# Kernel tuning notes

Measured on AMD Instinct MI355X. Metric: run time of the kernel, lower is better.

The kernel has to match this reference:

```python
import jax, jax.numpy as jnp
import numpy as np

TAU = 1.0      # temperature for gumbel-softmax
EPS = 1e-12    # F.normalize eps


def _l2norm(v, axis):
    n = jnp.sqrt(jnp.sum(v * v, axis=axis, keepdims=True))
    return v / jnp.maximum(n, EPS)


def setup_inputs() -> dict:
    key = jax.random.key(0)
    k1, k2, k3, k4 = jax.random.split(key, 4)
    b, c, h, w, n = 8, 512, 64, 64, 1024
    x = jax.random.normal(k1, (b, c, h, w), dtype=jnp.float32)
    centers = jax.random.normal(k2, (n, c), dtype=jnp.float32)          # VQ codebook
    clusters = jax.random.normal(k3, (n, c), dtype=jnp.float32)         # ClusterLookup param
    gumbel_noise = jax.random.gumbel(k4, (b, n, h, w), dtype=jnp.float32)
    return {"x": x, "centers": centers, "clusters": clusters, "gumbel_noise": gumbel_noise}


def reference(x, centers, clusters, gumbel_noise):
    # similarity logits: [b, n, h, w]
    inner = jnp.einsum('bchw,nc->bnhw', x, centers)
    # hard gumbel-softmax (straight-through) over code dim
    y_soft = jax.nn.softmax((inner + gumbel_noise) / TAU, axis=1)
    idx = jnp.argmax(y_soft, axis=1)                                     # [b, h, w]
    y_hard = jax.nn.one_hot(idx, centers.shape[0], axis=1, dtype=y_soft.dtype)
    one_hot = y_hard - jax.lax.stop_gradient(y_soft) + y_soft            # [b, n, h, w]
    # quantized features: codebook lookup expressed as einsum
    z_q = jnp.einsum('bnhw,nd->bdhw', one_hot, centers)                  # [b, c, h, w]
    # ClusterLookup(z_q, alpha=None, is_direct=False)
    nf = _l2norm(z_q, axis=1)
    ncl = _l2norm(clusters, axis=1)
    ip = jnp.einsum('bchw,nc->bnhw', nf, ncl)                            # cluster logits
    preds = jnp.argmax(ip, axis=1)                                       # [b, h, w] int
    probs = jax.nn.one_hot(preds, clusters.shape[0], axis=1, dtype=ip.dtype)
    cluster_loss = -jnp.mean(jnp.sum(probs * ip, axis=1))
    return (cluster_loss, preds, ip, z_q)
```

## Files before the change

### kernel.cpp

```cpp
#include <hip/hip_runtime.h>
#include <math.h>

#define C 512
#define HW 4096
#define N 1024
#define NPIX 32768
#define MARGIN 2.0f

typedef short s16x8 __attribute__((ext_vector_type(8)));
typedef float f32x4 __attribute__((ext_vector_type(4)));

__device__ inline unsigned short f2bf(float f) {
    unsigned int u = __float_as_uint(f);
    return (unsigned short)((u + 0x7FFFu + ((u >> 16) & 1u)) >> 16);
}
__device__ inline float h2f(unsigned short u) {
    _Float16 h; __builtin_memcpy(&h, &u, 2); return (float)h;
}
__device__ inline unsigned short f2h(float f) {
    _Float16 h = (_Float16)f; unsigned short u; __builtin_memcpy(&u, &h, 2); return u;
}
__device__ inline unsigned int mono(float v) {
    unsigned int u = __float_as_uint(v);
    return (u & 0x80000000u) ? ~u : (u | 0x80000000u);
}
__device__ inline void gload_lds16(const void* gsrc, void* ldst) {
    __builtin_amdgcn_global_load_lds(
        (const __attribute__((address_space(1))) unsigned int*)gsrc,
        (__attribute__((address_space(3))) unsigned int*)ldst, 16, 0, 0);
}

__global__ __launch_bounds__(64) void k_norms(const float* __restrict__ centers,
                                              const float* __restrict__ clusters,
                                              float* __restrict__ cnorm,
                                              float* __restrict__ clnorm) {
    int r = blockIdx.x;
    const float* src = (r < N) ? (centers + (size_t)r * C) : (clusters + (size_t)(r - N) * C);
    int lane = threadIdx.x;
    float s = 0.f;
    for (int k = lane; k < C; k += 64) { float v = src[k]; s += v * v; }
    #pragma unroll
    for (int m = 1; m < 64; m <<= 1) s += __shfl_xor(s, m, 64);
    if (lane == 0) {
        float nrm = sqrtf(s);
        if (nrm < 1e-12f) nrm = 1e-12f;
        if (r < N) cnorm[r] = nrm; else clnorm[r - N] = nrm;
    }
}

__global__ __launch_bounds__(256) void k_gemmM(const float* __restrict__ centers,
                                               const float* __restrict__ clusters,
                                               const float* __restrict__ cnorm,
                                               const float* __restrict__ clnorm,
                                               float* __restrict__ M) {
    __shared__ float as[32][68];
    __shared__ float bs[32][68];
    int tid = threadIdx.x;
    int tx = tid & 15, ty = tid >> 4;
    int i0 = blockIdx.x * 64, j0 = blockIdx.y * 64;
    int lrow = tid >> 2, lkq = (tid & 3) * 8;
    float acc[4][4] = {};
    for (int kc = 0; kc < C; kc += 32) {
        float4 a0 = *(const float4*)(centers + (size_t)(i0 + lrow) * C + kc + lkq);
        float4 a1 = *(const float4*)(centers + (size_t)(i0 + lrow) * C + kc + lkq + 4);
        float4 b0 = *(const float4*)(clusters + (size_t)(j0 + lrow) * C + kc + lkq);
        float4 b1 = *(const float4*)(clusters + (size_t)(j0 + lrow) * C + kc + lkq + 4);
        __syncthreads();
        as[lkq+0][lrow]=a0.x; as[lkq+1][lrow]=a0.y; as[lkq+2][lrow]=a0.z; as[lkq+3][lrow]=a0.w;
        as[lkq+4][lrow]=a1.x; as[lkq+5][lrow]=a1.y; as[lkq+6][lrow]=a1.z; as[lkq+7][lrow]=a1.w;
        bs[lkq+0][lrow]=b0.x; bs[lkq+1][lrow]=b0.y; bs[lkq+2][lrow]=b0.z; bs[lkq+3][lrow]=b0.w;
        bs[lkq+4][lrow]=b1.x; bs[lkq+5][lrow]=b1.y; bs[lkq+6][lrow]=b1.z; bs[lkq+7][lrow]=b1.w;
        __syncthreads();
        #pragma unroll
        for (int k = 0; k < 32; k += 4) {
            float av[4][4], bv[4][4];
            #pragma unroll
            for (int kk = 0; kk < 4; ++kk) {
                float4 ta = *(const float4*)&as[k+kk][tx*4];
                float4 tb = *(const float4*)&bs[k+kk][ty*4];
                av[kk][0]=ta.x; av[kk][1]=ta.y; av[kk][2]=ta.z; av[kk][3]=ta.w;
                bv[kk][0]=tb.x; bv[kk][1]=tb.y; bv[kk][2]=tb.z; bv[kk][3]=tb.w;
            }
            #pragma unroll
            for (int kk = 0; kk < 4; ++kk)
                #pragma unroll
                for (int ii = 0; ii < 4; ++ii)
                    #pragma unroll
                    for (int jj = 0; jj < 4; ++jj)
                        acc[ii][jj] = fmaf(av[kk][ii], bv[kk][jj], acc[ii][jj]);
        }
    }
    float rci[4], rcj[4];
    #pragma unroll
    for (int ii = 0; ii < 4; ++ii) rci[ii] = cnorm[i0 + tx*4 + ii];
    #pragma unroll
    for (int jj = 0; jj < 4; ++jj) rcj[jj] = clnorm[j0 + ty*4 + jj];
    #pragma unroll
    for (int ii = 0; ii < 4; ++ii)
        #pragma unroll
        for (int jj = 0; jj < 4; ++jj)
            M[(size_t)(i0 + tx*4 + ii) * N + (j0 + ty*4 + jj)] = acc[ii][jj] / (rci[ii] * rcj[jj]);
}

__global__ __launch_bounds__(256) void k_rowstat(const float* __restrict__ M,
                                                 float* __restrict__ rowmax,
                                                 int* __restrict__ rowarg) {
    __shared__ float sv[256];
    __shared__ int   sa[256];
    int i = blockIdx.x, tid = threadIdx.x;
    float bv = -INFINITY; int ba = 0;
    for (int j = tid; j < N; j += 256) {
        float v = M[(size_t)i * N + j];
        if (v > bv || (v == bv && j < ba)) { bv = v; ba = j; }
    }
    sv[tid] = bv; sa[tid] = ba;
    __syncthreads();
    for (int s = 128; s > 0; s >>= 1) {
        if (tid < s) {
            float v = sv[tid + s]; int a = sa[tid + s];
            if (v > sv[tid] || (v == sv[tid] && a < sa[tid])) { sv[tid] = v; sa[tid] = a; }
        }
        __syncthreads();
    }
    if (tid == 0) { rowmax[i] = sv[0]; rowarg[i] = sa[0]; }
}

__global__ __launch_bounds__(256) void k_prepT(const float* __restrict__ x,
                                               float* __restrict__ xT) {
    __shared__ float t[64][65];
    int bidx = blockIdx.x;
    int pt = bidx & 63, kt = (bidx >> 6) & 7, b = bidx >> 9;
    int r = threadIdx.x >> 4, c4 = (threadIdx.x & 15) * 4;
    const float* src = x + ((size_t)b * C + kt * 64) * HW + pt * 64;
    #pragma unroll
    for (int rr = 0; rr < 4; ++rr) {
        int row = rr * 16 + r;
        float4 v = *(const float4*)(src + (size_t)row * HW + c4);
        t[row][c4] = v.x; t[row][c4+1] = v.y; t[row][c4+2] = v.z; t[row][c4+3] = v.w;
    }
    __syncthreads();
    float* dst = xT + ((size_t)b * HW + pt * 64) * C + kt * 64;
    #pragma unroll
    for (int rr = 0; rr < 4; ++rr) {
        int row = rr * 16 + r;
        float4 v = { t[c4][row], t[c4+1][row], t[c4+2][row], t[c4+3][row] };
        *(float4*)(dst + (size_t)row * C + c4) = v;
    }
}

__global__ __launch_bounds__(64) void k_cenfrag(const float* __restrict__ centers,
                                                unsigned short* __restrict__ cenB) {
    int f = blockIdx.x;
    int nt = f >> 4, kt = f & 15;
    int lane = threadIdx.x;
    int r = lane & 15, g = lane >> 4;
    const float* src = centers + (size_t)(nt * 16 + r) * C + kt * 32 + g * 4;
    float4 lo = *(const float4*)src;
    float4 hi = *(const float4*)(src + 16);
    union { unsigned short us[8]; uint4 q; } u;
    u.us[0]=f2bf(lo.x); u.us[1]=f2bf(lo.y); u.us[2]=f2bf(lo.z); u.us[3]=f2bf(lo.w);
    u.us[4]=f2bf(hi.x); u.us[5]=f2bf(hi.y); u.us[6]=f2bf(hi.z); u.us[7]=f2bf(hi.w);
    *(uint4*)(cenB + ((size_t)f * 64 + lane) * 8) = u.q;
}

__global__ __launch_bounds__(256, 3) void k_fused(const float* __restrict__ xT,
                                                  const unsigned short* __restrict__ cenB,
                                                  const float* __restrict__ gumbel,
                                                  const float* __restrict__ centers,
                                                  int* __restrict__ idxb) {
    __shared__ unsigned short cen[2][8192];
    __shared__ unsigned long long pixkey[64];
    __shared__ unsigned int candlist[4][256];
    __shared__ int candcount[4];

    int tid = threadIdx.x;
    int lane = tid & 63, w = tid >> 6;
    int r = lane & 15, g = lane >> 4;

    int p0 = blockIdx.x * 64;
    int b = p0 >> 12, hw0 = p0 & (HW - 1);

    if (tid < 64) pixkey[tid] = 0ull;
    if (tid < 4) candcount[tid] = 0;

    {
        const char* src = (const char*)cenB + w * 4096 + lane * 16;
        char* dst = (char*)&cen[0][0] + w * 4096;
        #pragma unroll
        for (int i = 0; i < 4; ++i) gload_lds16(src + i * 1024, dst + i * 1024);
    }

    s16x8 a[16];
    {
        const float* xrow = xT + (size_t)(p0 + w * 16 + r) * C;
        #pragma unroll
        for (int kt = 0; kt < 16; ++kt) {
            float4 lo = *(const float4*)(xrow + kt * 32 + g * 4);
            float4 hi = *(const float4*)(xrow + kt * 32 + 16 + g * 4);
            s16x8 t;
            t[0]=(short)f2bf(lo.x); t[1]=(short)f2bf(lo.y); t[2]=(short)f2bf(lo.z); t[3]=(short)f2bf(lo.w);
            t[4]=(short)f2bf(hi.x); t[5]=(short)f2bf(hi.y); t[6]=(short)f2bf(hi.z); t[7]=(short)f2bf(hi.w);
            a[kt] = t;
        }
    }
    __syncthreads();

    const float* gpx = gumbel + (size_t)b * N * HW + hw0 + w * 16 + g * 4;
    float m4[4] = {-INFINITY, -INFINITY, -INFINITY, -INFINITY};
    int cur = 0;

    for (int tc = 0; tc < 8; ++tc) {
        unsigned int keepH[16];
        #pragma unroll
        for (int s = 0; s < 8; ++s) {
            int t = tc * 8 + s;
            if (t < 63) {
                const char* src = (const char*)cenB + (size_t)(t + 1) * 16384 + w * 4096 + lane * 16;
                char* dst = (char*)&cen[cur ^ 1][0] + w * 4096;
                #pragma unroll
                for (int i = 0; i < 4; ++i) gload_lds16(src + i * 1024, dst + i * 1024);
            }
            float4 gv = *(const float4*)(gpx + (size_t)(t * 16 + r) * HW);
            const s16x8* bp = (const s16x8*)&cen[cur][0] + lane;
            f32x4 acc0 = {0.f,0.f,0.f,0.f}, acc1 = {0.f,0.f,0.f,0.f};
            #pragma unroll
            for (int kt = 0; kt < 16; kt += 2) {
                acc0 = __builtin_amdgcn_mfma_f32_16x16x32_bf16(a[kt],   bp[kt*64],     acc0, 0,0,0);
                acc1 = __builtin_amdgcn_mfma_f32_16x16x32_bf16(a[kt+1], bp[(kt+1)*64], acc1, 0,0,0);
            }
            float v0 = acc0[0]+acc1[0]+gv.x, v1 = acc0[1]+acc1[1]+gv.y;
            float v2 = acc0[2]+acc1[2]+gv.z, v3 = acc0[3]+acc1[3]+gv.w;
            m4[0]=fmaxf(m4[0],v0); m4[1]=fmaxf(m4[1],v1);
            m4[2]=fmaxf(m4[2],v2); m4[3]=fmaxf(m4[3],v3);
            keepH[s*2]   = (unsigned int)f2h(v0) | ((unsigned int)f2h(v1) << 16);
            keepH[s*2+1] = (unsigned int)f2h(v2) | ((unsigned int)f2h(v3) << 16);
            __syncthreads();
            cur ^= 1;
        }
        #pragma unroll
        for (int s2 = 1; s2 < 16; s2 <<= 1) {
            #pragma unroll
            for (int j = 0; j < 4; ++j) m4[j] = fmaxf(m4[j], __shfl_xor(m4[j], s2, 64));
        }
        float thr[4];
        #pragma unroll
        for (int j = 0; j < 4; ++j) thr[j] = m4[j] - MARGIN;
        #pragma unroll
        for (int s = 0; s < 8; ++s) {
            int nn = ((tc * 8 + s) << 4) + r;
            #pragma unroll
            for (int j2 = 0; j2 < 2; ++j2) {
                unsigned int pk = keepH[s * 2 + j2];
                float lo = h2f((unsigned short)(pk & 0xFFFFu));
                float hi = h2f((unsigned short)(pk >> 16));
                if (lo >= thr[j2 * 2]) {
                    int pos = atomicAdd(&candcount[w], 1);
                    if (pos < 256) candlist[w][pos] =
                        (unsigned int)nn | ((unsigned int)(w * 16 + g * 4 + j2 * 2) << 10);
                }
                if (hi >= thr[j2 * 2 + 1]) {
                    int pos = atomicAdd(&candcount[w], 1);
                    if (pos < 256) candlist[w][pos] =
                        (unsigned int)nn | ((unsigned int)(w * 16 + g * 4 + j2 * 2 + 1) << 10);
                }
            }
        }
    }

    int cc = candcount[w]; if (cc > 256) cc = 256;
    int sl = lane & 15, cg = lane >> 4;
    for (int t0 = 0; t0 < cc; t0 += 4) {
        int c = t0 + cg;
        bool valid = c < cc;
        unsigned int e = candlist[w][valid ? c : 0];
        int n = (int)(e & 1023u), pl = (int)(e >> 10);
        const float* xr = xT + (size_t)(p0 + pl) * C;
        const float* cenr = centers + (size_t)n * C;
        float s = 0.f;
        #pragma unroll
        for (int m = 0; m < 8; ++m) {
            int G = sl + (m << 4);
            float4 xv = *(const float4*)(xr + (G << 2));
            float4 cv = *(const float4*)(cenr + (G << 2));
            s = fmaf(xv.x, cv.x, s); s = fmaf(xv.y, cv.y, s);
            s = fmaf(xv.z, cv.z, s); s = fmaf(xv.w, cv.w, s);
        }
        #pragma unroll
        for (int s2 = 1; s2 < 16; s2 <<= 1) s += __shfl_xor(s, s2, 64);
        if (valid && sl == 0) {
            float val = s + gumbel[((size_t)b * N + n) * HW + hw0 + pl];
            unsigned long long key = ((unsigned long long)mono(val) << 32) | (unsigned int)(1023 - n);
            atomicMax(&pixkey[pl], key);
        }
    }
    __syncthreads();
    if (tid < 64) idxb[p0 + tid] = 1023 - (int)(unsigned int)(pixkey[tid] & 0xFFFFFFFFull);
}

__global__ __launch_bounds__(256) void k_preds(const int* __restrict__ idxb,
                                               const float* __restrict__ rowmax,
                                               const int* __restrict__ rowarg,
                                               float* __restrict__ preds_out,
                                               float* __restrict__ partial) {
    __shared__ float sv[256];
    int gid = blockIdx.x * 256 + threadIdx.x;
    int i = idxb[gid];
    preds_out[gid] = (float)rowarg[i];
    sv[threadIdx.x] = rowmax[i];
    __syncthreads();
    for (int s = 128; s > 0; s >>= 1) {
        if (threadIdx.x < s) sv[threadIdx.x] += sv[threadIdx.x + s];
        __syncthreads();
    }
    if (threadIdx.x == 0) partial[blockIdx.x] = sv[0];
}

__global__ __launch_bounds__(256) void k_gather(const float* __restrict__ src, int ncols,
                                                const int* __restrict__ idx,
                                                float* __restrict__ dst) {
    __shared__ float rows[64][65];
    int tile = blockIdx.x;
    int col0 = blockIdx.y * 64;
    int tid = threadIdx.x;
    int lane = tid & 63, w = tid >> 6;
    int b = tile >> 6, hw0 = (tile & 63) << 6;
    #pragma unroll
    for (int r8 = 0; r8 < 16; ++r8) {
        int r = w * 16 + r8;
        int row = idx[tile * 64 + r];
        rows[r][lane] = src[(size_t)row * ncols + col0 + lane];
    }
    __syncthreads();
    #pragma unroll
    for (int jj = 0; jj < 16; ++jj) {
        int j = col0 + w * 16 + jj;
        dst[((size_t)b * ncols + j) * HW + hw0 + lane] = rows[lane][w * 16 + jj];
    }
}

__global__ __launch_bounds__(128) void k_loss(const float* __restrict__ partial,
                                              float* __restrict__ out) {
    __shared__ float sv[128];
    sv[threadIdx.x] = partial[threadIdx.x];
    __syncthreads();
    for (int s = 64; s > 0; s >>= 1) {
        if (threadIdx.x < s) sv[threadIdx.x] += sv[threadIdx.x + s];
        __syncthreads();
    }
    if (threadIdx.x == 0) out[0] = -(sv[0] / 32768.0f);
}

extern "C" void kernel_launch(void* const* d_in, const int* in_sizes, int n_in,
                              void* d_out, int out_size, void* d_ws, size_t ws_size,
                              hipStream_t stream) {
    const float* x        = (const float*)d_in[0];
    const float* centers  = (const float*)d_in[1];
    const float* clusters = (const float*)d_in[2];
    const float* gumbel   = (const float*)d_in[3];
    float* out = (float*)d_out;

    char* w = (char*)d_ws;
    int*   idxb    = (int*)w;
    float* cnorm   = (float*)(w + 131072);
    float* clnorm  = cnorm + 1024;
    float* rowmax  = clnorm + 1024;
    int*   rowarg  = (int*)(rowmax + 1024);
    float* partial = (float*)(rowarg + 1024);
    float* M       = (float*)(w + 262144);
    unsigned short* cenB = (unsigned short*)(w + 4456448);

    float* out_loss  = out;
    float* out_preds = out + 1;
    float* out_ip    = out + 1 + 32768;
    float* out_zq    = out + 1 + 32768 + (size_t)N * NPIX;

    float* xT = out_zq;

    k_norms  <<<2048, 64, 0, stream>>>(centers, clusters, cnorm, clnorm);
    k_gemmM  <<<dim3(16, 16), 256, 0, stream>>>(centers, clusters, cnorm, clnorm, M);
    k_rowstat<<<1024, 256, 0, stream>>>(M, rowmax, rowarg);
    k_cenfrag<<<1024, 64, 0, stream>>>(centers, cenB);
    k_prepT  <<<4096, 256, 0, stream>>>(x, xT);
    k_fused  <<<512, 256, 0, stream>>>(xT, cenB, gumbel, centers, idxb);
    k_preds  <<<128, 256, 0, stream>>>(idxb, rowmax, rowarg, out_preds, partial);
    k_gather <<<dim3(512, 16), 256, 0, stream>>>(M, N, idxb, out_ip);
    k_gather <<<dim3(512, 8),  256, 0, stream>>>(centers, C, idxb, out_zq);
    k_loss   <<<1, 128, 0, stream>>>(partial, out_loss);
}
```

Measured before the change: 272.3 us.

## Split codebook search across two blocks per pixel tile with global atomic argmax

The fused VQ kernel now splits the 1024-code search into two halves handled by separate blocks, doubling the grid to 1024 blocks. The per-pixel best key moves from shared memory into a global buffer that is zeroed in k_cenfrag, merged with atomicMax, and decoded in k_preds. The aim is more parallelism on a 512-block grid that underfills the GPU. It also raises the occupancy target to 4 and prefetches gumbel one step ahead, using explicit vmcnt waits and a raw s_barrier in place of __syncthreads. The cost is global atomics, xT fragments loaded twice, and the candidate margin now applied within each half only, so more candidates may be kept.

```diff
diff --git a/kernel.cpp b/kernel.cpp
--- a/kernel.cpp
+++ b/kernel.cpp
@@ -149,10 +149,12 @@
 }
 
 __global__ __launch_bounds__(64) void k_cenfrag(const float* __restrict__ centers,
-                                                unsigned short* __restrict__ cenB) {
+                                                unsigned short* __restrict__ cenB,
+                                                unsigned long long* __restrict__ pixbest) {
     int f = blockIdx.x;
+    int lane = threadIdx.x;
+    if (f < 512) pixbest[f * 64 + lane] = 0ull;
     int nt = f >> 4, kt = f & 15;
-    int lane = threadIdx.x;
     int r = lane & 15, g = lane >> 4;
     const float* src = centers + (size_t)(nt * 16 + r) * C + kt * 32 + g * 4;
     float4 lo = *(const float4*)src;
@@ -163,13 +165,12 @@
     *(uint4*)(cenB + ((size_t)f * 64 + lane) * 8) = u.q;
 }
 
-__global__ __launch_bounds__(256, 3) void k_fused(const float* __restrict__ xT,
+__global__ __launch_bounds__(256, 4) void k_fused(const float* __restrict__ xT,
                                                   const unsigned short* __restrict__ cenB,
                                                   const float* __restrict__ gumbel,
                                                   const float* __restrict__ centers,
-                                                  int* __restrict__ idxb) {
+                                                  unsigned long long* __restrict__ pixbest) {
     __shared__ unsigned short cen[2][8192];
-    __shared__ unsigned long long pixkey[64];
     __shared__ unsigned int candlist[4][256];
     __shared__ int candcount[4];
 
@@ -177,14 +178,15 @@
     int lane = tid & 63, w = tid >> 6;
     int r = lane & 15, g = lane >> 4;
 
-    int p0 = blockIdx.x * 64;
+    int blk = blockIdx.x;
+    int gr = blk & 1;
+    int p0 = (blk >> 1) * 64;
     int b = p0 >> 12, hw0 = p0 & (HW - 1);
 
-    if (tid < 64) pixkey[tid] = 0ull;
     if (tid < 4) candcount[tid] = 0;
 
     {
-        const char* src = (const char*)cenB + w * 4096 + lane * 16;
+        const char* src = (const char*)cenB + (size_t)(gr * 32) * 16384 + w * 4096 + lane * 16;
         char* dst = (char*)&cen[0][0] + w * 4096;
         #pragma unroll
         for (int i = 0; i < 4; ++i) gload_lds16(src + i * 1024, dst + i * 1024);
@@ -203,24 +205,27 @@
             a[kt] = t;
         }
     }
-    __syncthreads();
-
-    const float* gpx = gumbel + (size_t)b * N * HW + hw0 + w * 16 + g * 4;
+    const float* gpx = gumbel + ((size_t)b * N + (size_t)gr * 512) * HW + hw0 + w * 16 + g * 4;
+    float4 gv_c = *(const float4*)(gpx + (size_t)r * HW);
+    __syncthreads();
+
     float m4[4] = {-INFINITY, -INFINITY, -INFINITY, -INFINITY};
     int cur = 0;
 
-    for (int tc = 0; tc < 8; ++tc) {
+    for (int tc = 0; tc < 4; ++tc) {
         unsigned int keepH[16];
         #pragma unroll
         for (int s = 0; s < 8; ++s) {
             int t = tc * 8 + s;
-            if (t < 63) {
-                const char* src = (const char*)cenB + (size_t)(t + 1) * 16384 + w * 4096 + lane * 16;
+            if (t < 31) {
+                const char* src = (const char*)cenB + (size_t)(gr * 32 + t + 1) * 16384 + w * 4096 + lane * 16;
                 char* dst = (char*)&cen[cur ^ 1][0] + w * 4096;
                 #pragma unroll
                 for (int i = 0; i < 4; ++i) gload_lds16(src + i * 1024, dst + i * 1024);
             }
-            float4 gv = *(const float4*)(gpx + (size_t)(t * 16 + r) * HW);
+            __builtin_amdgcn_sched_barrier(0);
+            float4 gv_n = gv_c;
+            if (t < 31) gv_n = *(const float4*)(gpx + (size_t)((t + 1) * 16 + r) * HW);
             const s16x8* bp = (const s16x8*)&cen[cur][0] + lane;
             f32x4 acc0 = {0.f,0.f,0.f,0.f}, acc1 = {0.f,0.f,0.f,0.f};
             #pragma unroll
@@ -228,14 +233,18 @@
                 acc0 = __builtin_amdgcn_mfma_f32_16x16x32_bf16(a[kt],   bp[kt*64],     acc0, 0,0,0);
                 acc1 = __builtin_amdgcn_mfma_f32_16x16x32_bf16(a[kt+1], bp[(kt+1)*64], acc1, 0,0,0);
             }
-            float v0 = acc0[0]+acc1[0]+gv.x, v1 = acc0[1]+acc1[1]+gv.y;
-            float v2 = acc0[2]+acc1[2]+gv.z, v3 = acc0[3]+acc1[3]+gv.w;
+            float v0 = acc0[0]+acc1[0]+gv_c.x, v1 = acc0[1]+acc1[1]+gv_c.y;
+            float v2 = acc0[2]+acc1[2]+gv_c.z, v3 = acc0[3]+acc1[3]+gv_c.w;
             m4[0]=fmaxf(m4[0],v0); m4[1]=fmaxf(m4[1],v1);
             m4[2]=fmaxf(m4[2],v2); m4[3]=fmaxf(m4[3],v3);
             keepH[s*2]   = (unsigned int)f2h(v0) | ((unsigned int)f2h(v1) << 16);
             keepH[s*2+1] = (unsigned int)f2h(v2) | ((unsigned int)f2h(v3) << 16);
-            __syncthreads();
+            if (t < 31) asm volatile("s_waitcnt vmcnt(1)" ::: "memory");
+            else        asm volatile("s_waitcnt vmcnt(0)" ::: "memory");
+            __builtin_amdgcn_s_barrier();
+            __builtin_amdgcn_sched_barrier(0);
             cur ^= 1;
+            gv_c = gv_n;
         }
         #pragma unroll
         for (int s2 = 1; s2 < 16; s2 <<= 1) {
@@ -247,7 +256,7 @@
         for (int j = 0; j < 4; ++j) thr[j] = m4[j] - MARGIN;
         #pragma unroll
         for (int s = 0; s < 8; ++s) {
-            int nn = ((tc * 8 + s) << 4) + r;
+            int nn = ((gr * 32 + tc * 8 + s) << 4) + r;
             #pragma unroll
             for (int j2 = 0; j2 < 2; ++j2) {
                 unsigned int pk = keepH[s * 2 + j2];
@@ -290,21 +299,22 @@
         if (valid && sl == 0) {
             float val = s + gumbel[((size_t)b * N + n) * HW + hw0 + pl];
             unsigned long long key = ((unsigned long long)mono(val) << 32) | (unsigned int)(1023 - n);
-            atomicMax(&pixkey[pl], key);
-        }
-    }
-    __syncthreads();
-    if (tid < 64) idxb[p0 + tid] = 1023 - (int)(unsigned int)(pixkey[tid] & 0xFFFFFFFFull);
-}
-
-__global__ __launch_bounds__(256) void k_preds(const int* __restrict__ idxb,
+            atomicMax(&pixbest[p0 + pl], key);
+        }
+    }
+}
+
+__global__ __launch_bounds__(256) void k_preds(const unsigned long long* __restrict__ pixbest,
                                                const float* __restrict__ rowmax,
                                                const int* __restrict__ rowarg,
+                                               int* __restrict__ idxb,
                                                float* __restrict__ preds_out,
                                                float* __restrict__ partial) {
     __shared__ float sv[256];
     int gid = blockIdx.x * 256 + threadIdx.x;
-    int i = idxb[gid];
+    unsigned long long key = pixbest[gid];
+    int i = 1023 - (int)(unsigned int)(key & 0xFFFFFFFFull);
+    idxb[gid] = i;
     preds_out[gid] = (float)rowarg[i];
     sv[threadIdx.x] = rowmax[i];
     __syncthreads();
@@ -368,6 +378,7 @@
     float* partial = (float*)(rowarg + 1024);
     float* M       = (float*)(w + 262144);
     unsigned short* cenB = (unsigned short*)(w + 4456448);
+    unsigned long long* pixbest = (unsigned long long*)(w + 5505024);
 
     float* out_loss  = out;
     float* out_preds = out + 1;
@@ -379,10 +390,10 @@
     k_norms  <<<2048, 64, 0, stream>>>(centers, clusters, cnorm, clnorm);
     k_gemmM  <<<dim3(16, 16), 256, 0, stream>>>(centers, clusters, cnorm, clnorm, M);
     k_rowstat<<<1024, 256, 0, stream>>>(M, rowmax, rowarg);
-    k_cenfrag<<<1024, 64, 0, stream>>>(centers, cenB);
+    k_cenfrag<<<1024, 64, 0, stream>>>(centers, cenB, pixbest);
     k_prepT  <<<4096, 256, 0, stream>>>(x, xT);
-    k_fused  <<<512, 256, 0, stream>>>(xT, cenB, gumbel, centers, idxb);
-    k_preds  <<<128, 256, 0, stream>>>(idxb, rowmax, rowarg, out_preds, partial);
+    k_fused  <<<1024, 256, 0, stream>>>(xT, cenB, gumbel, centers, pixbest);
+    k_preds  <<<128, 256, 0, stream>>>(pixbest, rowmax, rowarg, idxb, out_preds, partial);
     k_gather <<<dim3(512, 16), 256, 0, stream>>>(M, N, idxb, out_ip);
     k_gather <<<dim3(512, 8),  256, 0, stream>>>(centers, C, idxb, out_zq);
     k_loss   <<<1, 128, 0, stream>>>(partial, out_loss);
```

Result: slower. 328.4 us (+20.6%).
